# Optimization experiments

Measured on AMD Instinct MI355X. Metric: run time of the kernel, lower is better.

The kernel has to match this reference:

```python
import jax, jax.numpy as jnp
import numpy as np

B, S, E, H = 4, 4096, 1024, 128

def setup_inputs() -> dict:
    key = jax.random.key(0)
    kx, kk, kq, kv = jax.random.split(key, 4)
    x = jax.random.normal(kx, (B, S, E), dtype=jnp.float32)
    # torch nn.Linear weights are [out_features, in_features]
    Wk = jax.random.normal(kk, (H, E), dtype=jnp.float32) * (E ** -0.5)
    Wq = jax.random.normal(kq, (H, E), dtype=jnp.float32) * (E ** -0.5)
    Wv = jax.random.normal(kv, (H, E), dtype=jnp.float32) * (E ** -0.5)
    return {"x": x, "Wk": Wk, "Wq": Wq, "Wv": Wv}

def reference(x, Wk, Wq, Wv):
    # projections: y = x @ W.T  (bias-free nn.Linear)
    k = jnp.einsum('bse,he->bsh', x, Wk)
    q = jnp.einsum('bse,he->bsh', x, Wq)
    v = jnp.einsum('bse,he->bsh', x, Wv)
    emb = x.shape[-1]
    # scores scaled by embedding_size**-0.5 (as in the source, not head_size)
    scores = jnp.einsum('bqh,bkh->bqk', q, k) * (emb ** -0.5)  # [B,S,S]
    # causal mask: positions j > i get -inf
    i = jnp.arange(scores.shape[-2])[:, None]
    j = jnp.arange(scores.shape[-1])[None, :]
    scores = jnp.where(j > i, jnp.float32(-jnp.inf), scores)
    probs = jax.nn.softmax(scores, axis=-1)
    # dropout is identity in eval mode
    out = jnp.einsum('bqk,bkh->bqh', probs, v)  # [B,S,H]
    return out
```

## Files before the change

### kernel.cpp

```cpp
#include <hip/hip_runtime.h>

typedef short bf16x8 __attribute__((ext_vector_type(8)));
typedef float f32x4 __attribute__((ext_vector_type(4)));

#define MFMA16(a, b, c) __builtin_amdgcn_mfma_f32_16x16x32_bf16(a, b, c, 0, 0, 0)

constexpr int Bn = 4, Sn = 4096, En = 1024, Hn = 128;
constexpr float CSCALE = 1.44269504089f * 0.03125f;

__device__ inline int sbase2(int qt2) {
    int g = (qt2 - 4) >> 2, r = (qt2 - 4) & 3;
    return 2 * g * g + 6 * g + r * (g + 2);
}
constexpr int NSLOT = 140;
constexpr int SLOT2_F = 16640;

__device__ inline unsigned short f2bf(float f) {
    unsigned int u = __builtin_bit_cast(unsigned int, f);
    u += 0x7fff + ((u >> 16) & 1);
    return (unsigned short)(u >> 16);
}

__device__ inline unsigned int pk2(float a, float b) {
    unsigned int ua = __builtin_bit_cast(unsigned int, a) + 0x8000u;
    unsigned int ub = __builtin_bit_cast(unsigned int, b) + 0x8000u;
    return __builtin_amdgcn_perm(ub, ua, 0x07060302u);
}

__device__ inline void gld16(const unsigned short* g, unsigned short* l) {
    __builtin_amdgcn_global_load_lds((const __attribute__((address_space(1))) void*)g,
                                     (__attribute__((address_space(3))) void*)l, 16, 0, 0);
}

__global__ __launch_bounds__(256) void prep_kernel(
    const float* __restrict__ Wk, const float* __restrict__ Wq, const float* __restrict__ Wv,
    unsigned short* __restrict__ wb, unsigned int* __restrict__ sched)
{
    int gy = blockIdx.x >> 5;
    const float* src = (gy == 0) ? Wq : (gy == 1) ? Wk : Wv;
    unsigned short* dst = wb + (size_t)gy * Hn * En;
    int t = (blockIdx.x & 31) * 256 + threadIdx.x;
    const float4* s4 = (const float4*)src;
    for (int i = 0; i < 4; ++i) {
        float4 v = s4[(size_t)t * 4 + i];
        uint2 w2 = { pk2(v.x, v.y), pk2(v.z, v.w) };
        *(uint2*)&dst[(size_t)t * 16 + i * 4] = w2;
    }
    if (blockIdx.x == 0) {
        const int bin = threadIdx.x;
        unsigned int it[3] = { 0xFFFFu, 0xFFFFu, 0xFFFFu };
        auto fullItem = [](int F) -> unsigned int {
            int b = F / 120, j = F % 120;
            int qt2 = 31, ch = 0;
            for (int q = 31; q >= 0; --q) {
                int nf = (q + 1) >> 2;
                if (j < nf) { qt2 = q; ch = j; break; }
                j -= nf;
            }
            return (unsigned int)(qt2 | (ch << 5) | (b << 8));
        };
        auto remItem = [](int v, int t) -> unsigned int {
            int b = t >> 3, i = t & 7;
            int qt2 = 4 * i + (v >> 1) - 1;
            int ch = (qt2 + 1) >> 2;
            return (unsigned int)(qt2 | (ch << 5) | (b << 8));
        };
        if (bin < 192) {
            it[0] = fullItem(2 * bin);
            it[1] = fullItem(2 * bin + 1);
        } else if (bin < 224) {
            int t2 = bin - 192;
            it[0] = fullItem(384 + 2 * t2);
            it[1] = fullItem(385 + 2 * t2);
            it[2] = remItem(2, t2);
        } else {
            int t2 = bin - 224;
            it[0] = fullItem(448 + t2);
            it[1] = remItem(6, t2);
            it[2] = remItem(4, t2);
        }
        for (int z = 0; z < 3; ++z) sched[z * 256 + bin] = it[z];
    }
}

__global__ __launch_bounds__(512, 2) void proj_kernel(
    const float* __restrict__ x, const unsigned short* __restrict__ wb,
    unsigned short* __restrict__ qb, unsigned short* __restrict__ kb,
    unsigned short* __restrict__ vbT)
{
    __shared__ __align__(16) unsigned short xs[2][64][64];
    __shared__ __align__(16) unsigned short wsm[2][384][64];

    const int m0 = blockIdx.x * 64;
    const int tid = threadIdx.x;
    const int lane = tid & 63, wave = tid >> 6;
    const int l15 = lane & 15, quad = lane >> 4;
    const int wn = wave * 48;

    f32x4 acc[4][3] = {};
    float4 xp[2];

    auto loadx = [&](int kc) {
        for (int p2 = 0; p2 < 2; ++p2) {
            int i = p2 * 512 + tid, row = i >> 4, c4 = (i & 15) * 4;
            xp[p2] = *(const float4*)&x[(size_t)(m0 + row) * En + kc * 64 + c4];
        }
    };
    auto writex = [&](int c) {
        for (int p2 = 0; p2 < 2; ++p2) {
            int i = p2 * 512 + tid, row = i >> 4, hc = i & 15;
            uint2 w2 = { pk2(xp[p2].x, xp[p2].y), pk2(xp[p2].z, xp[p2].w) };
            *(uint2*)((char*)&xs[c][0][0] + row * 128 + (((hc >> 1) ^ (row & 7)) << 4) + ((hc & 1) << 3)) = w2;
        }
    };
    auto issueW = [&](int kc, int c) {
        for (int j = 0; j < 6; ++j) {
            int seg = (wave * 6 + j) * 1024;
            int d = seg + (lane << 4);
            int row = d >> 7, chp = (d >> 4) & 7;
            gld16(wb + (size_t)row * En + kc * 64 + ((chp ^ (row & 7)) << 3),
                  (unsigned short*)((char*)&wsm[c][0][0] + seg));
        }
    };

    loadx(0);
    issueW(0, 0);
    writex(0);
    loadx(1);

    for (int kc = 0; kc < En / 64; ++kc) {
        const int c = kc & 1;
        __syncthreads();
        if (kc + 1 < En / 64) {
            issueW(kc + 1, c ^ 1);
            writex(c ^ 1);
            int kn = (kc + 2 < En / 64) ? kc + 2 : En / 64 - 1;
            loadx(kn);
        }
        bf16x8 xf[4][2], wf[3][2];
        for (int i = 0; i < 4; ++i)
            for (int kk = 0; kk < 2; ++kk) {
                int row = i * 16 + l15;
                int chn = (kk * 4 + quad) ^ (row & 7);
                xf[i][kk] = *(const bf16x8*)((char*)&xs[c][0][0] + row * 128 + (chn << 4));
            }
        for (int j = 0; j < 3; ++j)
            for (int kk = 0; kk < 2; ++kk) {
                int row = wn + j * 16 + l15;
                int chn = (kk * 4 + quad) ^ (row & 7);
                wf[j][kk] = *(const bf16x8*)((char*)&wsm[c][0][0] + row * 128 + (chn << 4));
            }
        for (int kk = 0; kk < 2; ++kk)
            for (int i = 0; i < 4; ++i)
                for (int j = 0; j < 3; ++j)
                    acc[i][j] = MFMA16(xf[i][kk], wf[j][kk], acc[i][j]);
    }

    for (int i = 0; i < 4; ++i) {
        int rowb = m0 + i * 16 + quad * 4;
        for (int j = 0; j < 3; ++j) {
            int gcol = wn + j * 16 + l15;
            int gy = gcol >> 7, col = gcol & 127;
            if (gy == 0) {
                for (int r = 0; r < 4; ++r)
                    qb[(size_t)(rowb + r) * Hn + col] = f2bf(acc[i][j][r] * CSCALE);
            } else if (gy == 1) {
                for (int r = 0; r < 4; ++r)
                    kb[(size_t)(rowb + r) * Hn + col] = f2bf(acc[i][j][r]);
            } else {
                int bb = rowb >> 12, ss = rowb & 4095;
                uint2 w2 = { pk2(acc[i][j][0], acc[i][j][1]), pk2(acc[i][j][2], acc[i][j][3]) };
                *(uint2*)&vbT[((size_t)(bb * 128 + col)) * Sn + ss] = w2;
            }
        }
    }
}

__global__ __launch_bounds__(256, 2) void attn_kernel(
    const unsigned short* __restrict__ qb, const unsigned short* __restrict__ kb,
    const unsigned short* __restrict__ vbT, float* __restrict__ out,
    float* __restrict__ part, const unsigned int* __restrict__ sched)
{
    __shared__ unsigned short ks[64][132];
    __shared__ unsigned short vt[128][68];
    __shared__ unsigned short ps[4][32][72];

    const unsigned int wi = sched[blockIdx.x];
    if (wi == 0xFFFFu) return;
    const int qt2 = (int)(wi & 31u);
    const int ch  = (int)((wi >> 5) & 7u);
    const int b   = (int)((wi >> 8) & 3u);
    const int T2  = 2 * qt2 + 2;
    const int nch = (qt2 + 4) >> 2;
    const int t0 = ch * 8;
    const int nloc = min(8, T2 - t0);
    const int q0 = qt2 * 128;

    const int tid = threadIdx.x;
    const int lane = tid & 63, wave = tid >> 6;
    const int l15 = lane & 15, quad = lane >> 4;

    const unsigned short* qg = qb + (size_t)(b * Sn + q0) * Hn;
    bf16x8 qf[2][4];
    for (int g = 0; g < 2; ++g)
        for (int f = 0; f < 4; ++f)
            qf[g][f] = *(const bf16x8*)&qg[(wave * 32 + g * 16 + l15) * Hn + f * 32 + quad * 8];

    f32x4 o[2][8] = {};
    float m_r[2] = { -INFINITY, -INFINITY }, l_r[2] = { 0.f, 0.f };

    const unsigned short* kg = kb + (size_t)b * Sn * Hn;
    const unsigned short* vg = vbT + (size_t)b * 128 * Sn;

    bf16x8 kreg[4], vreg[4];
    auto loadKV = [&](int gt) {
        int kt0 = gt * 64;
        for (int p4 = 0; p4 < 4; ++p4) {
            int i = p4 * 256 + tid;
            kreg[p4] = *(const bf16x8*)&kg[(size_t)(kt0 + (i >> 4)) * Hn + (i & 15) * 8];
            vreg[p4] = *(const bf16x8*)&vg[(size_t)(i >> 3) * Sn + kt0 + (i & 7) * 8];
        }
    };

    loadKV(t0);
    for (int tl = 0; tl < nloc; ++tl) {
        const int gt = t0 + tl;
        for (int p4 = 0; p4 < 4; ++p4) {
            int i = p4 * 256 + tid;
            *(bf16x8*)&ks[i >> 4][(i & 15) * 8] = kreg[p4];
            *(bf16x8*)&vt[i >> 3][(i & 7) * 8] = vreg[p4];
        }
        __syncthreads();
        if (tl + 1 < nloc) loadKV(gt + 1);

        float u[2][4][4];
        for (int nt = 0; nt < 4; ++nt) {
            f32x4 s0 = {}, s1 = {};
            for (int kk = 0; kk < 4; ++kk) {
                bf16x8 kf = *(const bf16x8*)&ks[nt * 16 + l15][kk * 32 + quad * 8];
                s0 = MFMA16(kf, qf[0][kk], s0);
                s1 = MFMA16(kf, qf[1][kk], s1);
            }
            for (int r = 0; r < 4; ++r) { u[0][nt][r] = s0[r]; u[1][nt][r] = s1[r]; }
        }
        if (gt >= 2 * qt2) {
            int kof = (gt - 2 * qt2) * 64;
            for (int g = 0; g < 2; ++g) {
                int qq = wave * 32 + g * 16 + l15;
                for (int nt = 0; nt < 4; ++nt)
                    for (int r = 0; r < 4; ++r)
                        if (kof + nt * 16 + quad * 4 + r > qq) u[g][nt][r] = -INFINITY;
            }
        }
        for (int g = 0; g < 2; ++g) {
            float mx = -INFINITY;
            for (int nt = 0; nt < 4; ++nt)
                for (int r = 0; r < 4; ++r) mx = fmaxf(mx, u[g][nt][r]);
            mx = fmaxf(mx, __shfl_xor(mx, 16));
            mx = fmaxf(mx, __shfl_xor(mx, 32));
            float mn = fmaxf(m_r[g], mx);
            float alpha = exp2f(m_r[g] - mn);
            m_r[g] = mn;
            float sum = 0.f;
            for (int nt = 0; nt < 4; ++nt)
                for (int r = 0; r < 4; ++r) {
                    float pv = exp2f(u[g][nt][r] - mn);
                    u[g][nt][r] = pv;
                    sum += pv;
                }
            sum += __shfl_xor(sum, 16);
            sum += __shfl_xor(sum, 32);
            l_r[g] = l_r[g] * alpha + sum;

            unsigned short* psrow = &ps[wave][g * 16 + l15][0];
            for (int nt = 0; nt < 4; ++nt) {
                uint2 w2 = { pk2(u[g][nt][0], u[g][nt][1]), pk2(u[g][nt][2], u[g][nt][3]) };
                *(uint2*)&psrow[nt * 16 + quad * 4] = w2;
            }
            for (int t = 0; t < 8; ++t) o[g][t] *= alpha;
        }

        for (int k2 = 0; k2 < 2; ++k2) {
            bf16x8 pf0 = *(const bf16x8*)&ps[wave][0 * 16 + l15][k2 * 32 + quad * 8];
            bf16x8 pf1 = *(const bf16x8*)&ps[wave][1 * 16 + l15][k2 * 32 + quad * 8];
            for (int t = 0; t < 8; ++t) {
                bf16x8 vf = *(const bf16x8*)&vt[t * 16 + l15][k2 * 32 + quad * 8];
                o[0][t] = MFMA16(vf, pf0, o[0][t]);
                o[1][t] = MFMA16(vf, pf1, o[1][t]);
            }
        }
        __syncthreads();
    }

    if (nch == 1) {
        for (int g = 0; g < 2; ++g) {
            float inv = 1.0f / l_r[g];
            float* og = out + (size_t)(b * Sn + q0 + wave * 32 + g * 16 + l15) * Hn;
            for (int t = 0; t < 8; ++t) {
                float4 st = { o[g][t][0] * inv, o[g][t][1] * inv, o[g][t][2] * inv, o[g][t][3] * inv };
                *(float4*)&og[t * 16 + quad * 4] = st;
            }
        }
    } else {
        float* P = part + (size_t)(b * NSLOT + sbase2(qt2) + ch) * SLOT2_F;
        for (int g = 0; g < 2; ++g) {
            int q = wave * 32 + g * 16 + l15;
            for (int t = 0; t < 8; ++t) {
                float4 st = { o[g][t][0], o[g][t][1], o[g][t][2], o[g][t][3] };
                *(float4*)&P[q * 128 + t * 16 + quad * 4] = st;
            }
            if (quad == 0) {
                P[16384 + q] = m_r[g];
                P[16512 + q] = l_r[g];
            }
        }
    }
}

__global__ __launch_bounds__(256) void merge_kernel(
    const float* __restrict__ part, float* __restrict__ out)
{
    const int qt2 = 4 + (blockIdx.x >> 1);
    const int half = blockIdx.x & 1;
    const int b = blockIdx.y;
    const int nch = (qt2 + 4) >> 2;
    const float* P0 = part + (size_t)(b * NSLOT + sbase2(qt2)) * SLOT2_F;
    const int q = half * 64 + (threadIdx.x >> 2);
    const int h0 = (threadIdx.x & 3) * 32;

    float m[8], w[8];
    float M = -INFINITY;
    for (int c = 0; c < nch; ++c) {
        m[c] = P0[(size_t)c * SLOT2_F + 16384 + q];
        M = fmaxf(M, m[c]);
    }
    float L = 0.f;
    for (int c = 0; c < nch; ++c) {
        w[c] = exp2f(m[c] - M);
        L += w[c] * P0[(size_t)c * SLOT2_F + 16512 + q];
    }
    float inv = 1.0f / L;

    float acc[32] = {};
    for (int c = 0; c < nch; ++c) {
        const float* Pq = P0 + (size_t)c * SLOT2_F + q * 128 + h0;
        for (int j = 0; j < 8; ++j) {
            float4 v = *(const float4*)&Pq[j * 4];
            acc[j * 4 + 0] += w[c] * v.x;
            acc[j * 4 + 1] += w[c] * v.y;
            acc[j * 4 + 2] += w[c] * v.z;
            acc[j * 4 + 3] += w[c] * v.w;
        }
    }
    float* og = out + (size_t)(b * Sn + qt2 * 128 + q) * Hn + h0;
    for (int j = 0; j < 8; ++j) {
        float4 st = { acc[j * 4 + 0] * inv, acc[j * 4 + 1] * inv,
                      acc[j * 4 + 2] * inv, acc[j * 4 + 3] * inv };
        *(float4*)&og[j * 4] = st;
    }
}

extern "C" void kernel_launch(void* const* d_in, const int* in_sizes, int n_in,
                              void* d_out, int out_size, void* d_ws, size_t ws_size,
                              hipStream_t stream)
{
    const float* x  = (const float*)d_in[0];
    const float* Wk = (const float*)d_in[1];
    const float* Wq = (const float*)d_in[2];
    const float* Wv = (const float*)d_in[3];
    float* out = (float*)d_out;

    unsigned short* qbuf  = (unsigned short*)d_ws;
    unsigned short* kbuf  = qbuf + (size_t)Bn * Sn * Hn;
    unsigned short* vbufT = kbuf + (size_t)Bn * Sn * Hn;
    unsigned short* wb    = vbufT + (size_t)Bn * Sn * Hn;
    unsigned int* sched   = (unsigned int*)(wb + (size_t)3 * Hn * En);
    float* part = (float*)(sched + 1024);

    prep_kernel<<<96, 256, 0, stream>>>(Wk, Wq, Wv, wb, sched);
    proj_kernel<<<256, 512, 0, stream>>>(x, wb, qbuf, kbuf, vbufT);
    attn_kernel<<<768, 256, 0, stream>>>(qbuf, kbuf, vbufT, out, part, sched);
    merge_kernel<<<dim3(56, Bn), 256, 0, stream>>>(part, out);
}
```

Baseline: 182.4 us.

## Split attention work across eight waves of 16 query rows each

The attention kernel now launches 512 threads per block, eight waves each owning 16 query rows, where before four waves each owned 32. Per-wave register state (Q fragments, output accumulators, score tiles) is halved and launch bounds are raised so more waves can stay resident, and K/V tile loads are spread over more threads. In exchange, each K fragment read from LDS now feeds only one MFMA instead of two, which doubles LDS read traffic per unit of math, and block-wide syncs now cover more waves.

```diff
diff --git a/kernel.cpp b/kernel.cpp
--- a/kernel.cpp
+++ b/kernel.cpp
@@ -176,14 +176,14 @@
     }
 }
 
-__global__ __launch_bounds__(256, 2) void attn_kernel(
+__global__ __launch_bounds__(512, 4) void attn_kernel(
     const unsigned short* __restrict__ qb, const unsigned short* __restrict__ kb,
     const unsigned short* __restrict__ vbT, float* __restrict__ out,
     float* __restrict__ part, const unsigned int* __restrict__ sched)
 {
     __shared__ unsigned short ks[64][132];
     __shared__ unsigned short vt[128][68];
-    __shared__ unsigned short ps[4][32][72];
+    __shared__ unsigned short ps[8][16][72];
 
     const unsigned int wi = sched[blockIdx.x];
     if (wi == 0xFFFFu) return;
@@ -201,118 +201,106 @@
     const int l15 = lane & 15, quad = lane >> 4;
 
     const unsigned short* qg = qb + (size_t)(b * Sn + q0) * Hn;
-    bf16x8 qf[2][4];
-    for (int g = 0; g < 2; ++g)
-        for (int f = 0; f < 4; ++f)
-            qf[g][f] = *(const bf16x8*)&qg[(wave * 32 + g * 16 + l15) * Hn + f * 32 + quad * 8];
-
-    f32x4 o[2][8] = {};
-    float m_r[2] = { -INFINITY, -INFINITY }, l_r[2] = { 0.f, 0.f };
+    bf16x8 qf[4];
+    for (int f = 0; f < 4; ++f)
+        qf[f] = *(const bf16x8*)&qg[(wave * 16 + l15) * Hn + f * 32 + quad * 8];
+
+    f32x4 o[8] = {};
+    float m_r = -INFINITY, l_r = 0.f;
 
     const unsigned short* kg = kb + (size_t)b * Sn * Hn;
     const unsigned short* vg = vbT + (size_t)b * 128 * Sn;
-
-    bf16x8 kreg[4], vreg[4];
+    unsigned short* psrow = &ps[wave][l15][0];
+
+    bf16x8 kreg[2], vreg[2];
     auto loadKV = [&](int gt) {
         int kt0 = gt * 64;
-        for (int p4 = 0; p4 < 4; ++p4) {
-            int i = p4 * 256 + tid;
-            kreg[p4] = *(const bf16x8*)&kg[(size_t)(kt0 + (i >> 4)) * Hn + (i & 15) * 8];
-            vreg[p4] = *(const bf16x8*)&vg[(size_t)(i >> 3) * Sn + kt0 + (i & 7) * 8];
+        for (int p = 0; p < 2; ++p) {
+            int i = p * 512 + tid;
+            kreg[p] = *(const bf16x8*)&kg[(size_t)(kt0 + (i >> 4)) * Hn + (i & 15) * 8];
+            vreg[p] = *(const bf16x8*)&vg[(size_t)(i >> 3) * Sn + kt0 + (i & 7) * 8];
         }
     };
 
     loadKV(t0);
     for (int tl = 0; tl < nloc; ++tl) {
         const int gt = t0 + tl;
-        for (int p4 = 0; p4 < 4; ++p4) {
-            int i = p4 * 256 + tid;
-            *(bf16x8*)&ks[i >> 4][(i & 15) * 8] = kreg[p4];
-            *(bf16x8*)&vt[i >> 3][(i & 7) * 8] = vreg[p4];
+        for (int p = 0; p < 2; ++p) {
+            int i = p * 512 + tid;
+            *(bf16x8*)&ks[i >> 4][(i & 15) * 8] = kreg[p];
+            *(bf16x8*)&vt[i >> 3][(i & 7) * 8] = vreg[p];
         }
         __syncthreads();
         if (tl + 1 < nloc) loadKV(gt + 1);
 
-        float u[2][4][4];
+        float u[4][4];
         for (int nt = 0; nt < 4; ++nt) {
-            f32x4 s0 = {}, s1 = {};
+            f32x4 s = {};
             for (int kk = 0; kk < 4; ++kk) {
                 bf16x8 kf = *(const bf16x8*)&ks[nt * 16 + l15][kk * 32 + quad * 8];
-                s0 = MFMA16(kf, qf[0][kk], s0);
-                s1 = MFMA16(kf, qf[1][kk], s1);
-            }
-            for (int r = 0; r < 4; ++r) { u[0][nt][r] = s0[r]; u[1][nt][r] = s1[r]; }
+                s = MFMA16(kf, qf[kk], s);
+            }
+            for (int r = 0; r < 4; ++r) u[nt][r] = s[r];
         }
         if (gt >= 2 * qt2) {
             int kof = (gt - 2 * qt2) * 64;
-            for (int g = 0; g < 2; ++g) {
-                int qq = wave * 32 + g * 16 + l15;
-                for (int nt = 0; nt < 4; ++nt)
-                    for (int r = 0; r < 4; ++r)
-                        if (kof + nt * 16 + quad * 4 + r > qq) u[g][nt][r] = -INFINITY;
-            }
-        }
-        for (int g = 0; g < 2; ++g) {
-            float mx = -INFINITY;
+            int qq = wave * 16 + l15;
             for (int nt = 0; nt < 4; ++nt)
-                for (int r = 0; r < 4; ++r) mx = fmaxf(mx, u[g][nt][r]);
-            mx = fmaxf(mx, __shfl_xor(mx, 16));
-            mx = fmaxf(mx, __shfl_xor(mx, 32));
-            float mn = fmaxf(m_r[g], mx);
-            float alpha = exp2f(m_r[g] - mn);
-            m_r[g] = mn;
-            float sum = 0.f;
-            for (int nt = 0; nt < 4; ++nt)
-                for (int r = 0; r < 4; ++r) {
-                    float pv = exp2f(u[g][nt][r] - mn);
-                    u[g][nt][r] = pv;
-                    sum += pv;
-                }
-            sum += __shfl_xor(sum, 16);
-            sum += __shfl_xor(sum, 32);
-            l_r[g] = l_r[g] * alpha + sum;
-
-            unsigned short* psrow = &ps[wave][g * 16 + l15][0];
-            for (int nt = 0; nt < 4; ++nt) {
-                uint2 w2 = { pk2(u[g][nt][0], u[g][nt][1]), pk2(u[g][nt][2], u[g][nt][3]) };
-                *(uint2*)&psrow[nt * 16 + quad * 4] = w2;
-            }
-            for (int t = 0; t < 8; ++t) o[g][t] *= alpha;
-        }
+                for (int r = 0; r < 4; ++r)
+                    if (kof + nt * 16 + quad * 4 + r > qq) u[nt][r] = -INFINITY;
+        }
+        float mx = -INFINITY;
+        for (int nt = 0; nt < 4; ++nt)
+            for (int r = 0; r < 4; ++r) mx = fmaxf(mx, u[nt][r]);
+        mx = fmaxf(mx, __shfl_xor(mx, 16));
+        mx = fmaxf(mx, __shfl_xor(mx, 32));
+        float mn = fmaxf(m_r, mx);
+        float alpha = exp2f(m_r - mn);
+        m_r = mn;
+        float sum = 0.f;
+        for (int nt = 0; nt < 4; ++nt)
+            for (int r = 0; r < 4; ++r) {
+                float pv = exp2f(u[nt][r] - mn);
+                u[nt][r] = pv;
+                sum += pv;
+            }
+        sum += __shfl_xor(sum, 16);
+        sum += __shfl_xor(sum, 32);
+        l_r = l_r * alpha + sum;
+
+        for (int nt = 0; nt < 4; ++nt) {
+            uint2 w2 = { pk2(u[nt][0], u[nt][1]), pk2(u[nt][2], u[nt][3]) };
+            *(uint2*)&psrow[nt * 16 + quad * 4] = w2;
+        }
+        for (int t = 0; t < 8; ++t) o[t] *= alpha;
 
         for (int k2 = 0; k2 < 2; ++k2) {
-            bf16x8 pf0 = *(const bf16x8*)&ps[wave][0 * 16 + l15][k2 * 32 + quad * 8];
-            bf16x8 pf1 = *(const bf16x8*)&ps[wave][1 * 16 + l15][k2 * 32 + quad * 8];
+            bf16x8 pf = *(const bf16x8*)&psrow[k2 * 32 + quad * 8];
             for (int t = 0; t < 8; ++t) {
                 bf16x8 vf = *(const bf16x8*)&vt[t * 16 + l15][k2 * 32 + quad * 8];
-                o[0][t] = MFMA16(vf, pf0, o[0][t]);
-                o[1][t] = MFMA16(vf, pf1, o[1][t]);
+                o[t] = MFMA16(vf, pf, o[t]);
             }
         }
         __syncthreads();
     }
 
     if (nch == 1) {
-        for (int g = 0; g < 2; ++g) {
-            float inv = 1.0f / l_r[g];
-            float* og = out + (size_t)(b * Sn + q0 + wave * 32 + g * 16 + l15) * Hn;
-            for (int t = 0; t < 8; ++t) {
-                float4 st = { o[g][t][0] * inv, o[g][t][1] * inv, o[g][t][2] * inv, o[g][t][3] * inv };
-                *(float4*)&og[t * 16 + quad * 4] = st;
-            }
+        float inv = 1.0f / l_r;
+        float* og = out + (size_t)(b * Sn + q0 + wave * 16 + l15) * Hn;
+        for (int t = 0; t < 8; ++t) {
+            float4 st = { o[t][0] * inv, o[t][1] * inv, o[t][2] * inv, o[t][3] * inv };
+            *(float4*)&og[t * 16 + quad * 4] = st;
         }
     } else {
         float* P = part + (size_t)(b * NSLOT + sbase2(qt2) + ch) * SLOT2_F;
-        for (int g = 0; g < 2; ++g) {
-            int q = wave * 32 + g * 16 + l15;
-            for (int t = 0; t < 8; ++t) {
-                float4 st = { o[g][t][0], o[g][t][1], o[g][t][2], o[g][t][3] };
-                *(float4*)&P[q * 128 + t * 16 + quad * 4] = st;
-            }
-            if (quad == 0) {
-                P[16384 + q] = m_r[g];
-                P[16512 + q] = l_r[g];
-            }
+        int q = wave * 16 + l15;
+        for (int t = 0; t < 8; ++t) {
+            float4 st = { o[t][0], o[t][1], o[t][2], o[t][3] };
+            *(float4*)&P[q * 128 + t * 16 + quad * 4] = st;
+        }
+        if (quad == 0) {
+            P[16384 + q] = m_r;
+            P[16512 + q] = l_r;
         }
     }
 }
@@ -379,6 +367,6 @@
 
     prep_kernel<<<96, 256, 0, stream>>>(Wk, Wq, Wv, wb, sched);
     proj_kernel<<<256, 512, 0, stream>>>(x, wb, qbuf, kbuf, vbufT);
-    attn_kernel<<<768, 256, 0, stream>>>(qbuf, kbuf, vbufT, out, part, sched);
+    attn_kernel<<<768, 512, 0, stream>>>(qbuf, kbuf, vbufT, out, part, sched);
     merge_kernel<<<dim3(56, Bn), 256, 0, stream>>>(part, out);
 }
```

New measurement: 184.4 us. No clear change (+1.1%).
